# Optimization experiments

Measured on AMD Instinct MI355X. Metric: run time of the kernel, lower is better.

Reference implementation:

```python
import jax, jax.numpy as jnp
import numpy as np

EPS = 1e-12
CLAMP = 1.0 - 1e-6


def _hamilton(a, b):
    r1, i1, j1, k1 = a
    r2, i2, j2, k2 = b
    return (r1 * r2 - i1 * i2 - j1 * j2 - k1 * k2,
            r1 * i2 + i1 * r2 + j1 * k2 - k1 * j2,
            r1 * j2 - i1 * k2 + j1 * r2 + k1 * i2,
            r1 * k2 + i1 * j2 - j1 * i2 + k1 * r2)


def _chained_prod(r, i, j, k):
    """Left-to-right Hamilton product along the last axis via tree reduction."""
    n = r.shape[-1]
    m = 1 << (n - 1).bit_length()  # next power of two
    if m != n:
        pad = [(0, 0)] * (r.ndim - 1) + [(0, m - n)]
        # pad with identity quaternion (1,0,0,0)
        r = jnp.pad(r, pad, constant_values=1.0)
        i = jnp.pad(i, pad)
        j = jnp.pad(j, pad)
        k = jnp.pad(k, pad)
    q = (r, i, j, k)
    while q[0].shape[-1] > 1:
        a = tuple(t[..., 0::2] for t in q)
        b = tuple(t[..., 1::2] for t in q)
        q = _hamilton(a, b)
    return tuple(t[..., 0] for t in q)


def reference(x, weight, bias):
    # x: (B, T, 4*C_in) laid out as [r | i | j | k]; weight: (C_out, C_in); bias: (C_out,)
    r, i, j, k = jnp.split(x, 4, axis=-1)  # each (B, T, C_in)
    norm_v = jnp.sqrt(i * i + j * j + k * k + EPS)
    theta = jnp.arccos(jnp.clip(r, -CLAMP, CLAMP))  # (B, T, C_in)
    # quaternion power: angle scaled by weight, shifted by bias -> (B, T, C_out, C_in)
    theta = weight * theta[..., None, :] + bias[:, None]
    mul = jnp.sin(theta) / norm_v[..., None, :]
    qr = jnp.cos(theta)
    qi = i[..., None, :] * mul
    qj = j[..., None, :] * mul
    qk = k[..., None, :] * mul
    # chained Hamilton product over C_in -> (B, T, C_out)
    pr, pi, pj, pk = _chained_prod(qr, qi, qj, qk)
    # quaternion normalize
    n = jnp.sqrt(pr * pr + pi * pi + pj * pj + pk * pk + EPS)
    return jnp.concatenate([pr / n, pi / n, pj / n, pk / n], axis=-1)  # (B, T, 4*C_out)


def setup_inputs() -> dict:
    key = jax.random.key(0)
    k1, k2, k3 = jax.random.split(key, 3)
    C_in, C_out = 64, 128
    x = jax.random.normal(k1, (16, 128, 4 * C_in), dtype=jnp.float32)
    a = float(np.sqrt(6.0 / (C_in + C_out)))  # xavier bound
    weight = jax.random.uniform(k2, (C_out, C_in), minval=-a, maxval=a, dtype=jnp.float32)
    bias = jax.random.uniform(k3, (C_out,), minval=-a, maxval=a, dtype=jnp.float32)
    return {"x": x, "weight": weight, "bias": bias}
```

## Files before the change

kernel.cpp:

```cpp
#include <hip/hip_runtime.h>
#include <math.h>


typedef float v2f __attribute__((ext_vector_type(2)));

#define C_IN   64
#define C_OUT  128
#define POS_PER_BLOCK 4
#define BLOCK  512
#define HALF   (C_IN / 2)
#define WSTR2  (C_OUT / 2 + 1)

#define INV_2PI 0.15915494309189535f

__global__ __launch_bounds__(BLOCK, 2) void qpu_kernel(
    const float* __restrict__ x,
    const float* __restrict__ weight,
    const float* __restrict__ bias,
    float* __restrict__ out,
    int P)
{
    __shared__ float  w_s[C_IN * WSTR2 * 2];
    __shared__ float4 pre[POS_PER_BLOCK][C_IN];
    __shared__ v2f    part[POS_PER_BLOCK][4][64];

    const int tid  = threadIdx.x;
    const int lane = tid & 63;
    const int wave = tid >> 6;
    const int sub  = wave >> 1;
    const int half = wave & 1;

    {
        const float4* w4 = (const float4*)weight;
        #pragma unroll
        for (int idx = tid; idx < (C_OUT * C_IN) / 4; idx += BLOCK) {
            const float4 v = w4[idx];
            const int o  = idx >> 4;
            const int c0 = (idx & 15) * 4;
            w_s[(c0 + 0) * (2 * WSTR2) + o] = v.x;
            w_s[(c0 + 1) * (2 * WSTR2) + o] = v.y;
            w_s[(c0 + 2) * (2 * WSTR2) + o] = v.z;
            w_s[(c0 + 3) * (2 * WSTR2) + o] = v.w;
        }
    }

    const int pos = blockIdx.x * POS_PER_BLOCK + sub;
    const bool valid = (pos < P);

    {
        const int t = tid & 127;
        if (valid && t < C_IN) {
            const int c = t;
            const float* xb = x + (size_t)pos * (4 * C_IN);
            const float r = xb[c];
            const float i = xb[C_IN + c];
            const float j = xb[2 * C_IN + c];
            const float k = xb[3 * C_IN + c];
            const float rc = fminf(fmaxf(r, -0.999999f), 0.999999f);
            const float th0 = acosf(rc);
            const float inv = rsqrtf(fmaf(i, i, fmaf(j, j, fmaf(k, k, 1e-12f))));
            pre[sub][c] = make_float4(th0, i * inv, j * inv, k * inv);
        }
    }
    __syncthreads();

    const v2f b2 = ((const v2f*)bias)[lane] * INV_2PI;
    const v2f* __restrict__ w2 = (const v2f*)w_s;

    v2f pr = 1.0f, pi = 0.0f, pj = 0.0f, pk = 0.0f;

    if (valid) {
        const int c0 = half * HALF;
        #pragma unroll 8
        for (int cc = 0; cc < HALF; ++cc) {
            const int c = c0 + cc;
            const float4 p4 = pre[sub][c];
            const v2f    w  = w2[c * WSTR2 + lane];
            const v2f    rev = w * (p4.x * INV_2PI) + b2;
            v2f s, ct;
            s.x  = __builtin_amdgcn_sinf(rev.x);
            s.y  = __builtin_amdgcn_sinf(rev.y);
            ct.x = __builtin_amdgcn_cosf(rev.x);
            ct.y = __builtin_amdgcn_cosf(rev.y);
            const v2f qi = p4.y * s;
            const v2f qj = p4.z * s;
            const v2f qk = p4.w * s;
            const v2f nr = pr * ct - pi * qi - pj * qj - pk * qk;
            const v2f ni = pr * qi + pi * ct + pj * qk - pk * qj;
            const v2f nj = pr * qj - pi * qk + pj * ct + pk * qi;
            const v2f nk = pr * qk + pi * qj - pj * qi + pk * ct;
            pr = nr; pi = ni; pj = nj; pk = nk;
        }
    }

    if (half == 1) {
        part[sub][0][lane] = pr;
        part[sub][1][lane] = pi;
        part[sub][2][lane] = pj;
        part[sub][3][lane] = pk;
    }
    __syncthreads();

    if (!valid || half == 1) return;

    const v2f Br = part[sub][0][lane];
    const v2f Bi = part[sub][1][lane];
    const v2f Bj = part[sub][2][lane];
    const v2f Bk = part[sub][3][lane];
    const v2f tr = pr * Br - pi * Bi - pj * Bj - pk * Bk;
    const v2f ti = pr * Bi + pi * Br + pj * Bk - pk * Bj;
    const v2f tj = pr * Bj - pi * Bk + pj * Br + pk * Bi;
    const v2f tk = pr * Bk + pi * Bj - pj * Bi + pk * Br;

    const v2f n2 = tr * tr + ti * ti + tj * tj + tk * tk + 1e-12f;
    v2f invn;
    invn.x = rsqrtf(n2.x);
    invn.y = rsqrtf(n2.y);

    float* ob = out + (size_t)pos * (4 * C_OUT);
    ((v2f*)(ob            ))[lane] = tr * invn;
    ((v2f*)(ob +     C_OUT))[lane] = ti * invn;
    ((v2f*)(ob + 2 * C_OUT))[lane] = tj * invn;
    ((v2f*)(ob + 3 * C_OUT))[lane] = tk * invn;
}

extern "C" void kernel_launch(void* const* d_in, const int* in_sizes, int n_in,
                              void* d_out, int out_size, void* d_ws, size_t ws_size,
                              hipStream_t stream) {
    const float* x      = (const float*)d_in[0];
    const float* weight = (const float*)d_in[1];
    const float* bias   = (const float*)d_in[2];
    float* out          = (float*)d_out;

    const int P = in_sizes[0] / (4 * C_IN);
    const int grid = (P + POS_PER_BLOCK - 1) / POS_PER_BLOCK;

    qpu_kernel<<<grid, BLOCK, 0, stream>>>(x, weight, bias, out, P);
}
```

Baseline: 67.67 us.

## Split C_in chain into four quarters per position and combine partial products

Each position's Hamilton-product chain over C_in is now split across four waves instead of two, so the block grows to 1024 threads and each wave walks a sequence of 16. The partial products from waves 1-3 go through shared memory and are folded in order by wave 0. The 1/(2π) scaling of theta is moved into the per-channel precompute. This shortens the serial dependency chain and raises parallelism, but it adds a longer serial combine on wave 0, more shared memory, and the launch bound of 8 may be unreachable at 1024 threads per block.

```diff
diff --git a/kernel.cpp b/kernel.cpp
--- a/kernel.cpp
+++ b/kernel.cpp
@@ -7,13 +7,14 @@
 #define C_IN   64
 #define C_OUT  128
 #define POS_PER_BLOCK 4
-#define BLOCK  512
-#define HALF   (C_IN / 2)
+#define NQ     4
+#define QLEN   (C_IN / NQ)
+#define BLOCK  (POS_PER_BLOCK * NQ * 64)
 #define WSTR2  (C_OUT / 2 + 1)
 
 #define INV_2PI 0.15915494309189535f
 
-__global__ __launch_bounds__(BLOCK, 2) void qpu_kernel(
+__global__ __launch_bounds__(BLOCK, 8) void qpu_kernel(
     const float* __restrict__ x,
     const float* __restrict__ weight,
     const float* __restrict__ bias,
@@ -22,13 +23,13 @@
 {
     __shared__ float  w_s[C_IN * WSTR2 * 2];
     __shared__ float4 pre[POS_PER_BLOCK][C_IN];
-    __shared__ v2f    part[POS_PER_BLOCK][4][64];
+    __shared__ v2f    part[POS_PER_BLOCK][NQ - 1][4][64];
 
     const int tid  = threadIdx.x;
     const int lane = tid & 63;
     const int wave = tid >> 6;
-    const int sub  = wave >> 1;
-    const int half = wave & 1;
+    const int sub  = wave >> 2;
+    const int q    = wave & 3;
 
     {
         const float4* w4 = (const float4*)weight;
@@ -48,7 +49,7 @@
     const bool valid = (pos < P);
 
     {
-        const int t = tid & 127;
+        const int t = tid & 255;
         if (valid && t < C_IN) {
             const int c = t;
             const float* xb = x + (size_t)pos * (4 * C_IN);
@@ -57,7 +58,7 @@
             const float j = xb[2 * C_IN + c];
             const float k = xb[3 * C_IN + c];
             const float rc = fminf(fmaxf(r, -0.999999f), 0.999999f);
-            const float th0 = acosf(rc);
+            const float th0 = acosf(rc) * INV_2PI;
             const float inv = rsqrtf(fmaf(i, i, fmaf(j, j, fmaf(k, k, 1e-12f))));
             pre[sub][c] = make_float4(th0, i * inv, j * inv, k * inv);
         }
@@ -70,13 +71,13 @@
     v2f pr = 1.0f, pi = 0.0f, pj = 0.0f, pk = 0.0f;
 
     if (valid) {
-        const int c0 = half * HALF;
-        #pragma unroll 8
-        for (int cc = 0; cc < HALF; ++cc) {
+        const int c0 = q * QLEN;
+        #pragma unroll 4
+        for (int cc = 0; cc < QLEN; ++cc) {
             const int c = c0 + cc;
             const float4 p4 = pre[sub][c];
             const v2f    w  = w2[c * WSTR2 + lane];
-            const v2f    rev = w * (p4.x * INV_2PI) + b2;
+            const v2f    rev = w * p4.x + b2;
             v2f s, ct;
             s.x  = __builtin_amdgcn_sinf(rev.x);
             s.y  = __builtin_amdgcn_sinf(rev.y);
@@ -93,35 +94,39 @@
         }
     }
 
-    if (half == 1) {
-        part[sub][0][lane] = pr;
-        part[sub][1][lane] = pi;
-        part[sub][2][lane] = pj;
-        part[sub][3][lane] = pk;
+    if (q != 0) {
+        part[sub][q - 1][0][lane] = pr;
+        part[sub][q - 1][1][lane] = pi;
+        part[sub][q - 1][2][lane] = pj;
+        part[sub][q - 1][3][lane] = pk;
     }
     __syncthreads();
 
-    if (!valid || half == 1) return;
+    if (!valid || q != 0) return;
 
-    const v2f Br = part[sub][0][lane];
-    const v2f Bi = part[sub][1][lane];
-    const v2f Bj = part[sub][2][lane];
-    const v2f Bk = part[sub][3][lane];
-    const v2f tr = pr * Br - pi * Bi - pj * Bj - pk * Bk;
-    const v2f ti = pr * Bi + pi * Br + pj * Bk - pk * Bj;
-    const v2f tj = pr * Bj - pi * Bk + pj * Br + pk * Bi;
-    const v2f tk = pr * Bk + pi * Bj - pj * Bi + pk * Br;
+    #pragma unroll
+    for (int qq = 0; qq < NQ - 1; ++qq) {
+        const v2f Br = part[sub][qq][0][lane];
+        const v2f Bi = part[sub][qq][1][lane];
+        const v2f Bj = part[sub][qq][2][lane];
+        const v2f Bk = part[sub][qq][3][lane];
+        const v2f tr = pr * Br - pi * Bi - pj * Bj - pk * Bk;
+        const v2f ti = pr * Bi + pi * Br + pj * Bk - pk * Bj;
+        const v2f tj = pr * Bj - pi * Bk + pj * Br + pk * Bi;
+        const v2f tk = pr * Bk + pi * Bj - pj * Bi + pk * Br;
+        pr = tr; pi = ti; pj = tj; pk = tk;
+    }
 
-    const v2f n2 = tr * tr + ti * ti + tj * tj + tk * tk + 1e-12f;
+    const v2f n2 = pr * pr + pi * pi + pj * pj + pk * pk + 1e-12f;
     v2f invn;
     invn.x = rsqrtf(n2.x);
     invn.y = rsqrtf(n2.y);
 
     float* ob = out + (size_t)pos * (4 * C_OUT);
-    ((v2f*)(ob            ))[lane] = tr * invn;
-    ((v2f*)(ob +     C_OUT))[lane] = ti * invn;
-    ((v2f*)(ob + 2 * C_OUT))[lane] = tj * invn;
-    ((v2f*)(ob + 3 * C_OUT))[lane] = tk * invn;
+    ((v2f*)(ob            ))[lane] = pr * invn;
+    ((v2f*)(ob +     C_OUT))[lane] = pi * invn;
+    ((v2f*)(ob + 2 * C_OUT))[lane] = pj * invn;
+    ((v2f*)(ob + 3 * C_OUT))[lane] = pk * invn;
 }
 
 extern "C" void kernel_launch(void* const* d_in, const int* in_sizes, int n_in,
```

Measured after the change: 67.19 us. About the same (-0.7%).
